# Optimization experiments

Hardware: AMD Instinct MI355X
Metric: run time of the kernel (lower is better)

The kernel has to match this reference:

```python
import jax, jax.numpy as jnp
import numpy as np
import math

N, C, W = 4, 768, 2048
H = 12            # num_attention_heads
D = C // H        # attention_head_size = 64
G = 4             # q/k/v groups


def grouped_conv1x1(x, w, b):
    # x: [N, C, W]; w: [G, C/G, C/G] (cout_per_g, cin_per_g); b: [C]
    xg = x.reshape(N, G, C // G, W)
    out = jnp.einsum('goc,ngcw->ngow', w, xg)       # [N, G, C/G, W]
    return out.reshape(N, C, W) + b[None, :, None]


def setup_inputs() -> dict:
    key = jax.random.key(0)
    ks = jax.random.split(key, 7)
    s = 1.0 / math.sqrt(C // G)
    return {
        'hidden_states': jax.random.normal(ks[0], (N, C, W), jnp.float32),
        'attention_mask': jnp.zeros((N, 1, 1, W), jnp.float32),
        'wq': jax.random.normal(ks[1], (G, C // G, C // G), jnp.float32) * s,
        'bq': jax.random.normal(ks[2], (C,), jnp.float32) * 0.02,
        'wk': jax.random.normal(ks[3], (G, C // G, C // G), jnp.float32) * s,
        'bk': jax.random.normal(ks[4], (C,), jnp.float32) * 0.02,
        'wv': jax.random.normal(ks[5], (G, C // G, C // G), jnp.float32) * s,
        'bv': jax.random.normal(ks[6], (C,), jnp.float32) * 0.02,
    }


def reference(hidden_states, attention_mask, wq, bq, wk, bk, wv, bv):
    q = grouped_conv1x1(hidden_states, wq, bq)       # [N, C, W]
    k = grouped_conv1x1(hidden_states, wk, bk)
    v = grouped_conv1x1(hidden_states, wv, bv)
    # transpose_for_scores_conv1d: [N,C,W] -> [N,H,W,D]
    q = q.reshape(N, H, D, W).transpose(0, 1, 3, 2)
    # transpose_key_for_scores_conv1d: [N,C,W] -> [N,H,D,W]
    k = k.reshape(N, H, D, W)
    v = v.reshape(N, H, D, W).transpose(0, 1, 3, 2)
    scores = jnp.einsum('nhqd,nhdk->nhqk', q, k) / math.sqrt(D)
    scores = scores + attention_mask                 # broadcast [N,1,1,W]
    probs = jax.nn.softmax(scores, axis=-1)          # dropout p=0 (eval)
    ctx = jnp.einsum('nhqk,nhkd->nhqd', probs, v)    # [N,H,W,D]
    # transpose_output_conv1d: [N,H,W,D] -> [N,C,W]
    return ctx.transpose(0, 1, 3, 2).reshape(N, C, W)
```

## Files before the change

kernel.cpp:

```cpp
#include <hip/hip_runtime.h>
#include <math.h>

typedef __attribute__((ext_vector_type(4))) float floatx4;
typedef __attribute__((ext_vector_type(8))) short shortx8;
typedef __attribute__((ext_vector_type(4))) short shortx4;

#define NB 4
#define CC 768
#define WW 2048
#define HH 12
#define DD 64
#define GG 4
#define CG 192
#define HPG 3
#define L2E 1.4426950408889634f
#define C18 0.18033688011112043f
#define MSH 11.541560327111707f
#define WSZ (GG * CG * CG)

__device__ __forceinline__ float fast_exp2(float x) {
    return __builtin_amdgcn_exp2f(x);
}

__device__ __forceinline__ short f2bf(float f) {
    union { float f; unsigned u; } v; v.f = f;
    unsigned r = v.u + 0x7fffu + ((v.u >> 16) & 1u);
    return (short)(r >> 16);
}

template<int CTRL>
__device__ __forceinline__ float dppror(float v) {
    return __int_as_float(__builtin_amdgcn_update_dpp(
        0, __float_as_int(v), CTRL, 0xf, 0xf, false));
}
__device__ __forceinline__ float rsum16(float v) {
    v += dppror<0x128>(v);
    v += dppror<0x124>(v);
    v += dppror<0x122>(v);
    v += dppror<0x121>(v);
    return v;
}

__device__ __forceinline__ void gl_lds16(const void* g, void* l) {
    __builtin_amdgcn_global_load_lds(
        (const __attribute__((address_space(1))) unsigned int*)g,
        (__attribute__((address_space(3))) unsigned int*)l, 16, 0, 0);
}

__global__ __launch_bounds__(256) void prep(
    const float* __restrict__ x,
    const float* __restrict__ wq, const float* __restrict__ wk,
    const float* __restrict__ wv,
    short* __restrict__ XTh, short* __restrict__ Wf)
{
    __shared__ short Th[64 * 72];
    const int tid = threadIdx.x;
    const int b   = blockIdx.x;

    if (b < 1536) {
        const int w0 = (b & 31) * 64;
        const int c0 = ((b >> 5) % 12) * 64;
        const int n  = b / 384;
        const int w  = tid & 63;
        const int cb = (tid >> 6) * 16;

        float xv[16];
        #pragma unroll
        for (int j = 0; j < 16; ++j)
            xv[j] = x[((size_t)n * CC + c0 + cb + j) * WW + w0 + w];

        shortx8 hi0, hi1;
        #pragma unroll
        for (int j = 0; j < 8; ++j) { hi0[j] = f2bf(xv[j]); hi1[j] = f2bf(xv[j + 8]); }
        *(shortx8*)&Th[w * 72 + cb]     = hi0;
        *(shortx8*)&Th[w * 72 + cb + 8] = hi1;
        __syncthreads();

        const int wr = tid >> 2;
        const int cc = (tid & 3) * 16;
        const size_t ro = ((size_t)n * WW + w0 + wr) * CC + c0 + cc;
        *(shortx8*)&XTh[ro]     = *(const shortx8*)&Th[wr * 72 + cc];
        *(shortx8*)&XTh[ro + 8] = *(const shortx8*)&Th[wr * 72 + cc + 8];
    } else {
        const int t = (b - 1536) * 256 + tid;
        const int g  = t / (CG * CG);
        const int r  = t - g * (CG * CG);
        const int o  = r / CG;
        const int k  = r - o * CG;
        const int off = (((g * 12 + (o >> 4)) * 6 + (k >> 5)) * 512)
                      + ((k >> 3) & 3) * 128 + (o & 15) * 8 + (k & 7);
        const float* src[3] = {wq, wk, wv};
        #pragma unroll
        for (int m = 0; m < 3; ++m)
            Wf[m * WSZ + off] = f2bf(src[m][t]);
    }
}

__global__ __launch_bounds__(256) void qkv_gemm(
    const short* __restrict__ XTh, const short* __restrict__ Wf,
    const float* __restrict__ bq, const float* __restrict__ bk,
    const float* __restrict__ bv,
    short* __restrict__ Qb, short* __restrict__ Kb, short* __restrict__ Vb)
{
    __shared__ __align__(16) char smem[26112];
    short* Xh_l = (short*)smem;

    const int lin  = blockIdx.x;
    const int xcd  = lin & 7;
    const int iw   = lin >> 3;
    const int mat  = iw % 3;
    const int tile = (iw / 3) * 8 + xcd;
    const int p0   = (tile & 31) * 64;
    const int g    = (tile >> 5) & 3;
    const int n    = tile >> 7;

    const int tid  = threadIdx.x;
    const int wid  = __builtin_amdgcn_readfirstlane(tid >> 6);
    const int lane = tid & 63;
    const int l15  = lane & 15;
    const int quad = lane >> 4;
    const int ob   = wid * 48;

    {
        const short* xhb = XTh + ((size_t)n * WW + p0) * CC + g * CG;
        #pragma unroll
        for (int rd = 0; rd < 6; ++rd) {
            const int Lb = rd * 256 + wid * 64;
            const int L  = Lb + lane;
            const int p  = (L * 2731) >> 16;
            const int sc = L - p * 24;
            const int ss = (sc & ~7) | ((sc & 7) ^ (p & 7));
            gl_lds16(xhb + (size_t)p * CC + ss * 8, &Xh_l[Lb * 8]);
        }
    }
    __syncthreads();

    floatx4 acc[3][4];
    #pragma unroll
    for (int mi = 0; mi < 3; ++mi)
        #pragma unroll
        for (int ni = 0; ni < 4; ++ni) acc[mi][ni] = (floatx4)0.0f;

    const short* wfm = Wf + (size_t)mat * WSZ + lane * 8;

    #pragma unroll
    for (int ks = 0; ks < 6; ++ks) {
        shortx8 ah[3], bh[4];
        #pragma unroll
        for (int mi = 0; mi < 3; ++mi)
            ah[mi] = *(const shortx8*)(wfm + (((g * 12 + wid * 3 + mi) * 6 + ks) << 9));
        #pragma unroll
        for (int ni = 0; ni < 4; ++ni) {
            const int p  = ni * 16 + l15;
            const int vp = (ks >> 1) * 8 + ((((ks & 1) * 4) + quad) ^ (p & 7));
            bh[ni] = *(const shortx8*)&Xh_l[(p * 24 + vp) * 8];
        }
        #pragma unroll
        for (int mi = 0; mi < 3; ++mi)
            #pragma unroll
            for (int ni = 0; ni < 4; ++ni)
                acc[mi][ni] = __builtin_amdgcn_mfma_f32_16x16x32_bf16(ah[mi], bh[ni], acc[mi][ni], 0, 0, 0);
    }

    const float* bias = (mat == 0) ? bq : (mat == 1) ? bk : bv;
    short* Y = (mat == 0) ? Qb : (mat == 1) ? Kb : Vb;

    __syncthreads();

    if (mat < 2) {
        short* T = (short*)smem;
        #pragma unroll
        for (int mi = 0; mi < 3; ++mi) {
            float4 b4 = *(const float4*)&bias[g * CG + ob + mi * 16 + quad * 4];
            const int o = ob + mi * 16 + quad * 4;
            #pragma unroll
            for (int ni = 0; ni < 4; ++ni) {
                const int p = ni * 16 + l15;
                T[p * 200 + o]     = f2bf(acc[mi][ni][0] + b4.x);
                T[p * 200 + o + 1] = f2bf(acc[mi][ni][1] + b4.y);
                T[p * 200 + o + 2] = f2bf(acc[mi][ni][2] + b4.z);
                T[p * 200 + o + 3] = f2bf(acc[mi][ni][3] + b4.w);
            }
        }
        __syncthreads();
        #pragma unroll
        for (int hc = 0; hc < HPG; ++hc) {
            const size_t nh = (size_t)n * HH + g * HPG + hc;
            #pragma unroll
            for (int half = 0; half < 2; ++half) {
                const int idx = tid + half * 256;
                const int p  = idx >> 3;
                const int dc = (idx & 7) * 8;
                *(shortx8*)&Y[(nh * WW + p0 + p) * DD + dc] =
                    *(const shortx8*)&T[p * 200 + hc * 64 + dc];
            }
        }
    } else {
        short* T = (short*)smem;
        #pragma unroll
        for (int mi = 0; mi < 3; ++mi) {
            float4 b4 = *(const float4*)&bias[g * CG + ob + mi * 16 + quad * 4];
            const int o = ob + mi * 16 + quad * 4;
            #pragma unroll
            for (int ni = 0; ni < 4; ++ni) {
                const int p = ni * 16 + l15;
                T[(o)     * 68 + p] = f2bf(acc[mi][ni][0] + b4.x);
                T[(o + 1) * 68 + p] = f2bf(acc[mi][ni][1] + b4.y);
                T[(o + 2) * 68 + p] = f2bf(acc[mi][ni][2] + b4.z);
                T[(o + 3) * 68 + p] = f2bf(acc[mi][ni][3] + b4.w);
            }
        }
        __syncthreads();
        #pragma unroll
        for (int pass = 0; pass < 6; ++pass) {
            const int idx = tid + pass * 256;
            const int o  = idx >> 3;
            const int pc = (idx & 7) * 8;
            const size_t nh = (size_t)n * HH + g * HPG + (o >> 6);
            const int d = o & 63;
            *(shortx8*)&Y[(nh * DD + d) * WW + p0 + pc] =
                *(const shortx8*)&T[o * 68 + pc];
        }
    }
}

#define PST 72
#define RST 65

__global__ __launch_bounds__(256) void attn_split(
    const short* __restrict__ Qb, const short* __restrict__ Kb,
    const short* __restrict__ Vb, const float* __restrict__ mask,
    float* __restrict__ out)
{
    __shared__ __align__(16) char smem[33792];
    short* Ks_l = (short*)smem;
    short* Vs_l = (short*)(smem + 8192);
    short* Pl   = (short*)(smem + 16384);
    float* Ml   = (float*)(smem + 25600);

    const int lin  = blockIdx.x;
    const int xcd  = lin & 7;
    const int slot = lin >> 3;
    const int pair = xcd * 6 + (slot >> 5);
    const int qt   = slot & 31;
    const int n    = pair / HH;
    const int h    = pair % HH;
    const int q0   = qt * 64;

    const int tid  = threadIdx.x;
    const int wid  = __builtin_amdgcn_readfirstlane(tid >> 6);
    const int lane = tid & 63;
    const int l15  = lane & 15;
    const int quad = lane >> 4;

    const size_t nh = (size_t)n * HH + h;
    const short* Kbase = Kb + nh * WW * DD;
    const short* Vbase = Vb + nh * DD * WW;

    {
        const float* mbase = mask + (size_t)n * WW;
        #pragma unroll
        for (int i = 0; i < WW / 256; ++i)
            Ml[tid + i * 256] = fmaf(mbase[tid + i * 256], L2E, -MSH);
    }

    shortx8 qf[2];
    {
        const short* qp = Qb + (nh * WW + q0 + wid * 16 + l15) * DD + quad * 8;
        qf[0] = *(const shortx8*)(qp);
        qf[1] = *(const shortx8*)(qp + 32);
    }

    floatx4 oacc[4];
    #pragma unroll
    for (int nn2 = 0; nn2 < 4; ++nn2) oacc[nn2] = (floatx4)0.0f;
    float lst[4] = {0.f, 0.f, 0.f, 0.f};

    short* Pw = Pl + wid * 16 * PST;

    for (int kt = 0; kt < WW / 64; ++kt) {
        const int k0 = kt * 64;

        #pragma unroll
        for (int t = 0; t < 2; ++t) {
            const int R  = wid * 16 + t * 8;
            const int r  = R + (lane >> 3);
            const int cg = (lane & 7) ^ (r & 7);
            gl_lds16(Kbase + (size_t)(k0 + r) * DD + cg * 8, &Ks_l[R * 64]);
            gl_lds16(Vbase + (size_t)r * WW + k0 + cg * 8, &Vs_l[R * 64]);
        }
        __syncthreads();

        shortx8 kf[4][2], vf[4][2];
        #pragma unroll
        for (int jj = 0; jj < 4; ++jj) {
            const int r = 16 * jj + l15;
            #pragma unroll
            for (int hf = 0; hf < 2; ++hf)
                kf[jj][hf] = *(const shortx8*)&Ks_l[r * 64 + (((hf * 4 + quad) ^ (r & 7)) * 8)];
        }
        #pragma unroll
        for (int nn2 = 0; nn2 < 4; ++nn2) {
            const int r = 16 * nn2 + l15;
            #pragma unroll
            for (int hf = 0; hf < 2; ++hf)
                vf[nn2][hf] = *(const shortx8*)&Vs_l[r * 64 + (((hf * 4 + quad) ^ (r & 7)) * 8)];
        }
        float mv2[4];
        #pragma unroll
        for (int jj = 0; jj < 4; ++jj)
            mv2[jj] = Ml[k0 + 16 * jj + l15];

        floatx4 sacc[4];
        #pragma unroll
        for (int jj = 0; jj < 4; ++jj) {
            sacc[jj] = (floatx4)0.0f;
            sacc[jj] = __builtin_amdgcn_mfma_f32_16x16x32_bf16(qf[0], kf[jj][0], sacc[jj], 0, 0, 0);
            sacc[jj] = __builtin_amdgcn_mfma_f32_16x16x32_bf16(qf[1], kf[jj][1], sacc[jj], 0, 0, 0);
        }

        #pragma unroll
        for (int jj = 0; jj < 4; ++jj) {
            #pragma unroll
            for (int r = 0; r < 4; ++r) {
                float p = fast_exp2(fmaf(sacc[jj][r], C18, mv2[jj]));
                lst[r] += p;
                Pw[(quad * 4 + r) * PST + 16 * jj + l15] = f2bf(p);
            }
        }

        shortx8 pf0 = *(const shortx8*)&Pw[l15 * PST + quad * 8];
        shortx8 pf1 = *(const shortx8*)&Pw[l15 * PST + 32 + quad * 8];

        #pragma unroll
        for (int nn2 = 0; nn2 < 4; ++nn2) {
            oacc[nn2] = __builtin_amdgcn_mfma_f32_16x16x32_bf16(pf0, vf[nn2][0], oacc[nn2], 0, 0, 0);
            oacc[nn2] = __builtin_amdgcn_mfma_f32_16x16x32_bf16(pf1, vf[nn2][1], oacc[nn2], 0, 0, 0);
        }
        __syncthreads();
    }

    float linv[4];
    #pragma unroll
    for (int r = 0; r < 4; ++r) linv[r] = 1.0f / rsum16(lst[r]);

    float* Ol = (float*)smem;
    #pragma unroll
    for (int nn2 = 0; nn2 < 4; ++nn2)
        #pragma unroll
        for (int r = 0; r < 4; ++r)
            Ol[(wid * 16 + quad * 4 + r) * RST + nn2 * 16 + l15] = oacc[nn2][r] * linv[r];
    __syncthreads();

    float* obase = out + (nh * DD) * WW + q0;
    #pragma unroll
    for (int it = 0; it < 4; ++it) {
        const int idx = tid + it * 256;
        const int q4 = (idx & 15) * 4;
        const int d  = idx >> 4;
        floatx4 v;
        #pragma unroll
        for (int i = 0; i < 4; ++i) v[i] = Ol[(q4 + i) * RST + d];
        *(floatx4*)&obase[(size_t)d * WW + q4] = v;
    }
}

extern "C" void kernel_launch(void* const* d_in, const int* in_sizes, int n_in,
                              void* d_out, int out_size, void* d_ws, size_t ws_size,
                              hipStream_t stream) {
    const float* x    = (const float*)d_in[0];
    const float* mask = (const float*)d_in[1];
    const float* wq   = (const float*)d_in[2];
    const float* bq   = (const float*)d_in[3];
    const float* wk   = (const float*)d_in[4];
    const float* bk   = (const float*)d_in[5];
    const float* wv   = (const float*)d_in[6];
    const float* bv   = (const float*)d_in[7];
    float* out = (float*)d_out;

    const size_t per = (size_t)NB * HH * WW * DD;
    short* Qb  = (short*)d_ws;
    short* Kb  = Qb + per;
    short* Vb  = Kb + per;
    short* XTh = Vb + per;
    short* Wfp = XTh + per;

    hipLaunchKernelGGL(prep, dim3(1536 + WSZ / 256), dim3(256), 0, stream,
                       x, wq, wk, wv, XTh, Wfp);
    hipLaunchKernelGGL(qkv_gemm, dim3(1536), dim3(256), 0, stream,
                       XTh, Wfp, bq, bk, bv, Qb, Kb, Vb);
    hipLaunchKernelGGL(attn_split, dim3(1536), dim3(256), 0, stream,
                       Qb, Kb, Vb, mask, out);
}
```

Before: 199.5 us.

## Double-buffer K/V tiles in LDS to overlap loads with compute

The attention kernel now keeps two LDS buffers each for the K and V tiles. It issues the global-to-LDS copy of tile kt+1 before working on tile kt, so the loads overlap the MFMA and softmax work and the barrier right after each load goes away. Row pointers and swizzled column offsets are hoisted out of the loop. LDS use per block grows, which may lower the number of resident blocks per CU.

```diff
diff --git a/kernel.cpp b/kernel.cpp
--- a/kernel.cpp
+++ b/kernel.cpp
@@ -232,11 +232,9 @@
     const short* __restrict__ Vb, const float* __restrict__ mask,
     float* __restrict__ out)
 {
-    __shared__ __align__(16) char smem[33792];
-    short* Ks_l = (short*)smem;
-    short* Vs_l = (short*)(smem + 8192);
-    short* Pl   = (short*)(smem + 16384);
-    float* Ml   = (float*)(smem + 25600);
+    __shared__ __align__(16) char smem[50176];
+    short* Pl = (short*)(smem + 32768);
+    float* Ml = (float*)(smem + 41984);
 
     const int lin  = blockIdx.x;
     const int xcd  = lin & 7;
@@ -278,18 +276,36 @@
 
     short* Pw = Pl + wid * 16 * PST;
 
+    const int r0  = wid * 16 + (lane >> 3);
+    const int r1  = r0 + 8;
+    const int cg0 = (lane & 7) ^ (r0 & 7);
+    const int cg1 = (lane & 7) ^ (r1 & 7);
+    const short* kp0 = Kbase + (size_t)r0 * DD + cg0 * 8;
+    const short* kp1 = Kbase + (size_t)r1 * DD + cg1 * 8;
+    const short* vp0 = Vbase + (size_t)r0 * WW + cg0 * 8;
+    const short* vp1 = Vbase + (size_t)r1 * WW + cg1 * 8;
+    const int KR0 = (wid * 16) * 64, KR1 = (wid * 16 + 8) * 64;
+
+    #define STAGE(j, bb)                                                      \
+        do {                                                                  \
+            short* ksd = (short*)(smem + (bb) * 8192);                        \
+            short* vsd = (short*)(smem + 16384 + (bb) * 8192);                \
+            gl_lds16(kp0 + (size_t)(j) * 64 * DD, ksd + KR0);                 \
+            gl_lds16(kp1 + (size_t)(j) * 64 * DD, ksd + KR1);                 \
+            gl_lds16(vp0 + (j) * 64, vsd + KR0);                              \
+            gl_lds16(vp1 + (j) * 64, vsd + KR1);                              \
+        } while (0)
+
+    STAGE(0, 0);
+    __syncthreads();
+
     for (int kt = 0; kt < WW / 64; ++kt) {
+        const int bb = kt & 1;
+        if (kt + 1 < WW / 64) STAGE(kt + 1, 1 - bb);
+
+        const short* Ks_l = (const short*)(smem + bb * 8192);
+        const short* Vs_l = (const short*)(smem + 16384 + bb * 8192);
         const int k0 = kt * 64;
-
-        #pragma unroll
-        for (int t = 0; t < 2; ++t) {
-            const int R  = wid * 16 + t * 8;
-            const int r  = R + (lane >> 3);
-            const int cg = (lane & 7) ^ (r & 7);
-            gl_lds16(Kbase + (size_t)(k0 + r) * DD + cg * 8, &Ks_l[R * 64]);
-            gl_lds16(Vbase + (size_t)r * WW + k0 + cg * 8, &Vs_l[R * 64]);
-        }
-        __syncthreads();
 
         shortx8 kf[4][2], vf[4][2];
         #pragma unroll
@@ -339,6 +355,7 @@
         }
         __syncthreads();
     }
+    #undef STAGE
 
     float linv[4];
     #pragma unroll
```

Result: faster. 194.9 us (-2.3%).
